# Optimization experiments

Measured on AMD Instinct MI355X. Metric: run time of the kernel, lower is better.

The kernel has to match this reference:

```python
import jax, jax.numpy as jnp
import numpy as np

B, E, F_DIM, D = 32, 16, 64, 512  # batch, extra dim, fea_dim, input_dim
EXP = 4                            # feed-forward expansion
EPS = 1e-5


def _layernorm(x, g, b):
    m = jnp.mean(x, axis=-1, keepdims=True)
    v = jnp.mean(jnp.square(x - m), axis=-1, keepdims=True)
    return (x - m) * jax.lax.rsqrt(v + EPS) * g + b


def setup_inputs() -> dict:
    key = jax.random.key(0)
    ks = jax.random.split(key, 12)
    s = 1.0 / np.sqrt(D)
    inp = {
        "x": jax.random.normal(ks[0], (B, E, F_DIM, D), jnp.float32),
        "ln1_g": jnp.ones((D,), jnp.float32),
        "ln1_b": jnp.zeros((D,), jnp.float32),
        "Wq": jax.random.uniform(ks[1], (D, D), jnp.float32, -s, s),
        "bq": jax.random.uniform(ks[2], (D,), jnp.float32, -s, s),
        "Wk": jax.random.uniform(ks[3], (D, D), jnp.float32, -s, s),
        "bk": jax.random.uniform(ks[4], (D,), jnp.float32, -s, s),
        "Wv": jax.random.uniform(ks[5], (D, D), jnp.float32, -s, s),
        "bv": jax.random.uniform(ks[6], (D,), jnp.float32, -s, s),
        "wn_g": jnp.ones((F_DIM,), jnp.float32),
        "wn_b": jnp.zeros((F_DIM,), jnp.float32),
        "ln2_g": jnp.ones((D,), jnp.float32),
        "ln2_b": jnp.zeros((D,), jnp.float32),
        "W1": jax.random.uniform(ks[7], (D, EXP * D), jnp.float32, -s, s),
        "b1": jax.random.uniform(ks[8], (EXP * D,), jnp.float32, -s, s),
        "W2": jax.random.uniform(ks[9], (EXP * D, D), jnp.float32, -1.0 / np.sqrt(EXP * D), 1.0 / np.sqrt(EXP * D)),
        "b2": jax.random.uniform(ks[10], (D,), jnp.float32, -1.0 / np.sqrt(EXP * D), 1.0 / np.sqrt(EXP * D)),
    }
    return inp


def reference(x, ln1_g, ln1_b, Wq, bq, Wk, bk, Wv, bv, wn_g, wn_b, ln2_g, ln2_b, W1, b1, W2, b2):
    # --- Residual 1: LN -> feature multi-head attention (dropout = identity) ---
    h = _layernorm(x, ln1_g, ln1_b)                       # [B,E,F,D]
    q = h @ Wq + bq
    k = h @ Wk + bk
    v = h @ Wv + bv
    energy = jnp.einsum('beqd,bekd->beqk', q, k)          # [B,E,F,F]
    # LayerNorm over the key axis of the raw scores (the fusion-breaking op)
    energy = _layernorm(energy, wn_g, wn_b)
    att = jax.nn.softmax(energy / jnp.sqrt(jnp.float32(D)), axis=-1)
    attn_out = jnp.einsum('beal,belv->beav', att, v)      # [B,E,F,D]
    x = x + attn_out
    # --- Residual 2: LN -> FFN (Linear -> Linear, no activation) ---
    h2 = _layernorm(x, ln2_g, ln2_b)
    ff = (h2 @ W1 + b1) @ W2 + b2
    return x + ff
```

## Files before the change

### kernel.cpp

```cpp
#include <hip/hip_runtime.h>
#include <hip/hip_bf16.h>


#define D_DIM 512
#define NROWS 32768
#define NBE   512

typedef __attribute__((ext_vector_type(8))) short bf16x8;
typedef __attribute__((ext_vector_type(4))) float f32x4;

typedef const __attribute__((address_space(1))) unsigned g_u32;
typedef __attribute__((address_space(3))) unsigned lds_u32;

__device__ __forceinline__ short f2bf(float f) {
  union { float f; unsigned u; } c; c.f = f;
  unsigned u = c.u;
  unsigned r = (u + 0x7FFFu + ((u >> 16) & 1u)) >> 16;
  return (short)r;
}
__device__ __forceinline__ float bf2f(short s) {
  union { unsigned u; float f; } c; c.u = ((unsigned)(unsigned short)s) << 16;
  return c.f;
}

__global__ __launch_bounds__(256) void wconvT(const float* __restrict__ W,
                                              short* __restrict__ Wt,
                                              int K, int N) {
  __shared__ float tile[32][33];
  const int t = threadIdx.x;
  const int r  = t >> 3;
  const int c4 = (t & 7) * 4;
  const long k0 = (long)blockIdx.y * 32;
  const long n0 = (long)blockIdx.x * 32;
  float4 v = *(const float4*)&W[(k0 + r) * N + n0 + c4];
  tile[r][c4 + 0] = v.x; tile[r][c4 + 1] = v.y;
  tile[r][c4 + 2] = v.z; tile[r][c4 + 3] = v.w;
  __syncthreads();
  union { short sh[4]; int2 v; } o;
#pragma unroll
  for (int j = 0; j < 4; ++j) o.sh[j] = f2bf(tile[c4 + j][r]);
  *(int2*)&Wt[(n0 + r) * K + k0 + c4] = o.v;
}

__global__ __launch_bounds__(256) void ln_kernel(const float* __restrict__ x,
                                                 const float* __restrict__ gam,
                                                 const float* __restrict__ bet,
                                                 short* __restrict__ h) {
  const int t = threadIdx.x;
  const long row = (long)blockIdx.x * 4 + (t >> 6);
  const int lane = t & 63;
  const float* xr = x + row * D_DIM + lane * 8;
  float4 a = *(const float4*)xr;
  float4 b = *(const float4*)(xr + 4);
  float xs[8] = {a.x, a.y, a.z, a.w, b.x, b.y, b.z, b.w};
  float s = 0.f, ss = 0.f;
#pragma unroll
  for (int j = 0; j < 8; ++j) { s += xs[j]; ss += xs[j] * xs[j]; }
#pragma unroll
  for (int m = 1; m < 64; m <<= 1) {
    s  += __shfl_xor(s, m);
    ss += __shfl_xor(ss, m);
  }
  float mean = s * (1.f / D_DIM);
  float var  = ss * (1.f / D_DIM) - mean * mean;
  float rstd = rsqrtf(var + 1e-5f);
  union { short sh[8]; int4 v; } o;
#pragma unroll
  for (int j = 0; j < 8; ++j) {
    int d = lane * 8 + j;
    o.sh[j] = f2bf((xs[j] - mean) * rstd * gam[d] + bet[d]);
  }
  *(int4*)&h[row * D_DIM + lane * 8] = o.v;
}

template <int OUT_BF16, int RESID>
__global__ __launch_bounds__(512, 2) void gemm256(
    const short* __restrict__ A, const short* __restrict__ Bt,
    const float* __restrict__ bias0, const float* __restrict__ bias1,
    const float* __restrict__ bias2,
    void* __restrict__ out0, void* __restrict__ out1, void* __restrict__ out2,
    const float* __restrict__ resid, int K, int nsplit) {
  extern __shared__ short smem[];
  short* As = smem;
  short* Bs = smem + 3 * 8192;

  const int t = threadIdx.x;
  const int wave = t >> 6, lane = t & 63;
  const int lr = lane & 15, g = lane >> 4;
  const int wr = wave >> 2, wc = wave & 3;

  const int gx = gridDim.x;
  const int nwg = gx * gridDim.y;
  const int hid = blockIdx.y * gx + blockIdx.x;
  const int lid = (hid & 7) * (nwg >> 3) + (hid >> 3);
  const int m0 = (lid / gx) * 256;
  const int n0 = (lid % gx) * 256;

  const int seg = n0 / nsplit;
  const int ncol0 = n0 - seg * nsplit;
  const float* bias = seg == 0 ? bias0 : (seg == 1 ? bias1 : bias2);
  void* outp = seg == 0 ? out0 : (seg == 1 ? out1 : out2);

  const int srow = lane & 15;
  const int scol = (lane >> 4) * 8;
  const short* gA0 = &A[(long)(m0 + wave * 32 + srow) * K + scol];
  const short* gB0 = &Bt[(long)(n0 + wave * 32 + srow) * K + scol];
  const long rstep = 16L * K;

#define STAGE_A(bufi, kk)                                                      \
  do {                                                                         \
    __builtin_amdgcn_global_load_lds((g_u32*)(gA0 + (kk)),                     \
        (lds_u32*)(As + (bufi) * 8192 + (wave * 2) * 512), 16, 0, 0);          \
    __builtin_amdgcn_global_load_lds((g_u32*)(gA0 + rstep + (kk)),             \
        (lds_u32*)(As + (bufi) * 8192 + (wave * 2 + 1) * 512), 16, 0, 0);      \
  } while (0)
#define STAGE_B(bufi, kk)                                                      \
  do {                                                                         \
    __builtin_amdgcn_global_load_lds((g_u32*)(gB0 + (kk)),                     \
        (lds_u32*)(Bs + (bufi) * 8192 + (wave * 2) * 512), 16, 0, 0);          \
    __builtin_amdgcn_global_load_lds((g_u32*)(gB0 + rstep + (kk)),             \
        (lds_u32*)(Bs + (bufi) * 8192 + (wave * 2 + 1) * 512), 16, 0, 0);      \
  } while (0)

  f32x4 acc[8][4];
  const f32x4 vzero = {0.f, 0.f, 0.f, 0.f};
#pragma unroll
  for (int mi = 0; mi < 8; ++mi)
#pragma unroll
    for (int ni = 0; ni < 4; ++ni) acc[mi][ni] = vzero;

  const int nt = K >> 5;
  STAGE_A(0, 0);  STAGE_B(0, 0);
  STAGE_A(1, 32); STAGE_B(1, 32);

  int cur = 0, stg = 2;
  const int fo = lane * 8;
  for (int T = 0; T < nt; ++T) {
    if (T < nt - 1) asm volatile("s_waitcnt vmcnt(4)" ::: "memory");
    else            asm volatile("s_waitcnt vmcnt(0)" ::: "memory");
    asm volatile("s_barrier" ::: "memory");

    const short* sA = As + cur * 8192;
    const short* sB = Bs + cur * 8192;
    const int kof = (T + 2) * 32;
    const bool stage_more = (T + 2 < nt);

    bf16x8 af[4], bfr[4];
#pragma unroll
    for (int i = 0; i < 4; ++i)
      af[i] = *(const bf16x8*)&sA[(wr * 8 + i) * 512 + fo];
#pragma unroll
    for (int i = 0; i < 4; ++i)
      bfr[i] = *(const bf16x8*)&sB[(wc * 4 + i) * 512 + fo];
    if (stage_more) STAGE_A(stg, kof);
    asm volatile("s_barrier" ::: "memory");
    __builtin_amdgcn_sched_barrier(0);
    __builtin_amdgcn_s_setprio(1);
#pragma unroll
    for (int mi = 0; mi < 4; ++mi)
#pragma unroll
      for (int ni = 0; ni < 4; ++ni)
        acc[mi][ni] = __builtin_amdgcn_mfma_f32_16x16x32_bf16(af[mi], bfr[ni], acc[mi][ni], 0, 0, 0);
    __builtin_amdgcn_s_setprio(0);
    __builtin_amdgcn_sched_barrier(0);
    asm volatile("s_barrier" ::: "memory");

#pragma unroll
    for (int i = 0; i < 4; ++i)
      af[i] = *(const bf16x8*)&sA[(wr * 8 + 4 + i) * 512 + fo];
    if (stage_more) STAGE_B(stg, kof);
    asm volatile("s_barrier" ::: "memory");
    __builtin_amdgcn_sched_barrier(0);
    __builtin_amdgcn_s_setprio(1);
#pragma unroll
    for (int mi = 0; mi < 4; ++mi)
#pragma unroll
      for (int ni = 0; ni < 4; ++ni)
        acc[4 + mi][ni] = __builtin_amdgcn_mfma_f32_16x16x32_bf16(af[mi], bfr[ni], acc[4 + mi][ni], 0, 0, 0);
    __builtin_amdgcn_s_setprio(0);
    __builtin_amdgcn_sched_barrier(0);

    cur = cur == 2 ? 0 : cur + 1;
    stg = stg == 2 ? 0 : stg + 1;
  }
#undef STAGE_A
#undef STAGE_B

#pragma unroll
  for (int ni = 0; ni < 4; ++ni) {
    const int col = ncol0 + wc * 64 + ni * 16 + lr;
    const float bv = bias[col];
#pragma unroll
    for (int mi = 0; mi < 8; ++mi) {
#pragma unroll
      for (int r = 0; r < 4; ++r) {
        const long row = m0 + wr * 128 + mi * 16 + g * 4 + r;
        float val = acc[mi][ni][r] + bv;
        if (RESID) val += resid[row * (long)nsplit + col];
        if (OUT_BF16) ((short*)outp)[row * (long)nsplit + col] = f2bf(val);
        else          ((float*)outp)[row * (long)nsplit + col] = val;
      }
    }
  }
}

__global__ __launch_bounds__(256) void attn_kernel(
    const short* __restrict__ q, const short* __restrict__ k,
    const short* __restrict__ v, const float* __restrict__ x,
    const float* __restrict__ wn_g, const float* __restrict__ wn_b,
    const float* __restrict__ ln2_g, const float* __restrict__ ln2_b,
    float* __restrict__ x1, short* __restrict__ h2) {
  __shared__ float att_s[64][68];
  const int t = threadIdx.x;
  const int wave = t >> 6, lane = t & 63;
  const int lr = lane & 15, g = lane >> 4;
  const long base = (long)blockIdx.x * 64;
  const long qoff = base * D_DIM;

  const f32x4 vzero = {0.f, 0.f, 0.f, 0.f};
  f32x4 acc[4];
#pragma unroll
  for (int nt = 0; nt < 4; ++nt) acc[nt] = vzero;

  for (int ks = 0; ks < 16; ++ks) {
    const int kc = ks * 32 + g * 8;
    bf16x8 afr = *(const bf16x8*)&q[qoff + (long)(wave * 16 + lr) * D_DIM + kc];
#pragma unroll
    for (int nt = 0; nt < 4; ++nt) {
      bf16x8 bfr = *(const bf16x8*)&k[qoff + (long)(nt * 16 + lr) * D_DIM + kc];
      acc[nt] = __builtin_amdgcn_mfma_f32_16x16x32_bf16(afr, bfr, acc[nt], 0, 0, 0);
    }
  }

  const float scale = 0.044194173824159216f;
#pragma unroll
  for (int r = 0; r < 4; ++r) {
    float s = 0.f, ss = 0.f;
#pragma unroll
    for (int nt = 0; nt < 4; ++nt) { float e = acc[nt][r]; s += e; ss += e * e; }
#pragma unroll
    for (int m = 1; m < 16; m <<= 1) { s += __shfl_xor(s, m); ss += __shfl_xor(ss, m); }
    float mean = s * (1.f / 64);
    float var  = ss * (1.f / 64) - mean * mean;
    float rstd = rsqrtf(var + 1e-5f);
    float e[4]; float mx = -1e30f;
#pragma unroll
    for (int nt = 0; nt < 4; ++nt) {
      int col = nt * 16 + lr;
      e[nt] = ((acc[nt][r] - mean) * rstd * wn_g[col] + wn_b[col]) * scale;
      mx = fmaxf(mx, e[nt]);
    }
#pragma unroll
    for (int m = 1; m < 16; m <<= 1) mx = fmaxf(mx, __shfl_xor(mx, m));
    float se = 0.f;
#pragma unroll
    for (int nt = 0; nt < 4; ++nt) { e[nt] = expf(e[nt] - mx); se += e[nt]; }
#pragma unroll
    for (int m = 1; m < 16; m <<= 1) se += __shfl_xor(se, m);
    float inv = 1.f / se;
#pragma unroll
    for (int nt = 0; nt < 4; ++nt)
      att_s[wave * 16 + 4 * g + r][nt * 16 + lr] = e[nt] * inv;
  }
  __syncthreads();

  const int d0 = lane * 8;
  float accp[16][8];
#pragma unroll
  for (int qi = 0; qi < 16; ++qi)
#pragma unroll
    for (int j = 0; j < 8; ++j) accp[qi][j] = 0.f;

  for (int kk0 = 0; kk0 < 64; kk0 += 4) {
    float vf[4][8];
#pragma unroll
    for (int kc = 0; kc < 4; ++kc) {
      bf16x8 vv = *(const bf16x8*)&v[qoff + (long)(kk0 + kc) * D_DIM + d0];
#pragma unroll
      for (int j = 0; j < 8; ++j) vf[kc][j] = bf2f(vv[j]);
    }
#pragma unroll
    for (int qi = 0; qi < 16; ++qi) {
      float4 a4 = *(const float4*)&att_s[wave * 16 + qi][kk0];
#pragma unroll
      for (int j = 0; j < 8; ++j) {
        accp[qi][j] += a4.x * vf[0][j];
        accp[qi][j] += a4.y * vf[1][j];
        accp[qi][j] += a4.z * vf[2][j];
        accp[qi][j] += a4.w * vf[3][j];
      }
    }
  }

  float g2v[8], b2v[8];
#pragma unroll
  for (int j = 0; j < 8; ++j) { g2v[j] = ln2_g[d0 + j]; b2v[j] = ln2_b[d0 + j]; }

#pragma unroll
  for (int qi = 0; qi < 16; ++qi) {
    const long row = base + wave * 16 + qi;
    const float* xr = x + row * D_DIM + d0;
    float4 x0 = *(const float4*)xr;
    float4 xb = *(const float4*)(xr + 4);
    accp[qi][0] += x0.x; accp[qi][1] += x0.y;
    accp[qi][2] += x0.z; accp[qi][3] += x0.w;
    accp[qi][4] += xb.x; accp[qi][5] += xb.y;
    accp[qi][6] += xb.z; accp[qi][7] += xb.w;
    float* po = x1 + row * D_DIM + d0;
    *(float4*)po       = make_float4(accp[qi][0], accp[qi][1], accp[qi][2], accp[qi][3]);
    *(float4*)(po + 4) = make_float4(accp[qi][4], accp[qi][5], accp[qi][6], accp[qi][7]);
    float s = 0.f, ss = 0.f;
#pragma unroll
    for (int j = 0; j < 8; ++j) { s += accp[qi][j]; ss += accp[qi][j] * accp[qi][j]; }
#pragma unroll
    for (int m = 1; m < 64; m <<= 1) { s += __shfl_xor(s, m); ss += __shfl_xor(ss, m); }
    float mean = s * (1.f / D_DIM);
    float var  = ss * (1.f / D_DIM) - mean * mean;
    float rstd = rsqrtf(var + 1e-5f);
    union { short sh[8]; int4 v; } o;
#pragma unroll
    for (int j = 0; j < 8; ++j)
      o.sh[j] = f2bf((accp[qi][j] - mean) * rstd * g2v[j] + b2v[j]);
    *(int4*)&h2[row * D_DIM + d0] = o.v;
  }
}

extern "C" void kernel_launch(void* const* d_in, const int* in_sizes, int n_in,
                              void* d_out, int out_size, void* d_ws, size_t ws_size,
                              hipStream_t stream) {
  (void)in_sizes; (void)n_in; (void)out_size; (void)ws_size;
  const float* x     = (const float*)d_in[0];
  const float* ln1_g = (const float*)d_in[1];
  const float* ln1_b = (const float*)d_in[2];
  const float* Wq    = (const float*)d_in[3];
  const float* bq    = (const float*)d_in[4];
  const float* Wk    = (const float*)d_in[5];
  const float* bk    = (const float*)d_in[6];
  const float* Wv    = (const float*)d_in[7];
  const float* bv    = (const float*)d_in[8];
  const float* wn_g  = (const float*)d_in[9];
  const float* wn_b  = (const float*)d_in[10];
  const float* ln2_g = (const float*)d_in[11];
  const float* ln2_b = (const float*)d_in[12];
  const float* W1    = (const float*)d_in[13];
  const float* b1    = (const float*)d_in[14];
  const float* W2    = (const float*)d_in[15];
  const float* b2    = (const float*)d_in[16];
  float* out = (float*)d_out;

  char* ws = (char*)d_ws;
  short* h   = (short*)(ws);
  short* qb  = (short*)(ws + (size_t)32  * 1024 * 1024);
  short* kb  = (short*)(ws + (size_t)64  * 1024 * 1024);
  short* vb  = (short*)(ws + (size_t)96  * 1024 * 1024);
  short* ff1 = (short*)(ws + (size_t)32  * 1024 * 1024);
  short* Wqt = (short*)(ws + (size_t)160 * 1024 * 1024);
  short* Wkt = Wqt + 512 * 512;
  short* Wvt = Wkt + 512 * 512;
  short* W1t = Wvt + 512 * 512;
  short* W2t = W1t + 512 * 2048;

  const size_t lds_bytes = 3 * 8192 * 2 * 2;
  (void)hipFuncSetAttribute((const void*)gemm256<1, 0>,
      hipFuncAttributeMaxDynamicSharedMemorySize, (int)lds_bytes);
  (void)hipFuncSetAttribute((const void*)gemm256<0, 1>,
      hipFuncAttributeMaxDynamicSharedMemorySize, (int)lds_bytes);

  wconvT<<<dim3(512 / 32, 512 / 32),  256, 0, stream>>>(Wq, Wqt, 512, 512);
  wconvT<<<dim3(512 / 32, 512 / 32),  256, 0, stream>>>(Wk, Wkt, 512, 512);
  wconvT<<<dim3(512 / 32, 512 / 32),  256, 0, stream>>>(Wv, Wvt, 512, 512);
  wconvT<<<dim3(2048 / 32, 512 / 32), 256, 0, stream>>>(W1, W1t, 512, 2048);
  wconvT<<<dim3(512 / 32, 2048 / 32), 256, 0, stream>>>(W2, W2t, 2048, 512);

  ln_kernel<<<NROWS / 4, 256, 0, stream>>>(x, ln1_g, ln1_b, h);

  dim3 gqkv(1536 / 256, NROWS / 256);
  gemm256<1, 0><<<gqkv, 512, lds_bytes, stream>>>(h, Wqt, bq, bk, bv,
                                                  qb, kb, vb, nullptr, 512, 512);

  attn_kernel<<<NBE, 256, 0, stream>>>(qb, kb, vb, x, wn_g, wn_b,
                                       ln2_g, ln2_b, out, h);

  dim3 gff1(2048 / 256, NROWS / 256);
  gemm256<1, 0><<<gff1, 512, lds_bytes, stream>>>(h, W1t, b1, b1, b1,
                                                  ff1, ff1, ff1, nullptr, 512, 2048);

  dim3 gff2(512 / 256, NROWS / 256);
  gemm256<0, 1><<<gff2, 512, lds_bytes, stream>>>(ff1, W2t, b2, b2, b2,
                                                  out, out, out, out, 2048, 512);
}
```

Measured before the change: 543.2 us.

## Simplify GEMM main loop to single-phase staging and vectorize epilogue via LDS

Restructures the GEMM K-loop so the next tile's A and B loads are issued together right after the barrier, and all 8x4 MFMAs run in one phase. This removes the interleaved half-tile barriers and setprio scheduling. The epilogue now stages each 16-row accumulator slab through per-wave LDS, so residual reads and output writes become contiguous 16-byte vector accesses instead of scattered scalar stores. The trade-off is more live fragment registers (8 A fragments), less fine-grained overlap of loads with MFMA, and a possible hazard: the staging loads are issued into buffer stg before other waves may have finished reading it.

```diff
diff --git a/kernel.cpp b/kernel.cpp
--- a/kernel.cpp
+++ b/kernel.cpp
@@ -140,45 +140,25 @@
     else            asm volatile("s_waitcnt vmcnt(0)" ::: "memory");
     asm volatile("s_barrier" ::: "memory");
 
+    if (T + 2 < nt) {
+      STAGE_A(stg, (T + 2) * 32);
+      STAGE_B(stg, (T + 2) * 32);
+    }
+
     const short* sA = As + cur * 8192;
     const short* sB = Bs + cur * 8192;
-    const int kof = (T + 2) * 32;
-    const bool stage_more = (T + 2 < nt);
-
-    bf16x8 af[4], bfr[4];
-#pragma unroll
-    for (int i = 0; i < 4; ++i)
+    bf16x8 af[8], bfr[4];
+#pragma unroll
+    for (int i = 0; i < 8; ++i)
       af[i] = *(const bf16x8*)&sA[(wr * 8 + i) * 512 + fo];
 #pragma unroll
     for (int i = 0; i < 4; ++i)
       bfr[i] = *(const bf16x8*)&sB[(wc * 4 + i) * 512 + fo];
-    if (stage_more) STAGE_A(stg, kof);
-    asm volatile("s_barrier" ::: "memory");
-    __builtin_amdgcn_sched_barrier(0);
-    __builtin_amdgcn_s_setprio(1);
-#pragma unroll
-    for (int mi = 0; mi < 4; ++mi)
+#pragma unroll
+    for (int mi = 0; mi < 8; ++mi)
 #pragma unroll
       for (int ni = 0; ni < 4; ++ni)
         acc[mi][ni] = __builtin_amdgcn_mfma_f32_16x16x32_bf16(af[mi], bfr[ni], acc[mi][ni], 0, 0, 0);
-    __builtin_amdgcn_s_setprio(0);
-    __builtin_amdgcn_sched_barrier(0);
-    asm volatile("s_barrier" ::: "memory");
-
-#pragma unroll
-    for (int i = 0; i < 4; ++i)
-      af[i] = *(const bf16x8*)&sA[(wr * 8 + 4 + i) * 512 + fo];
-    if (stage_more) STAGE_B(stg, kof);
-    asm volatile("s_barrier" ::: "memory");
-    __builtin_amdgcn_sched_barrier(0);
-    __builtin_amdgcn_s_setprio(1);
-#pragma unroll
-    for (int mi = 0; mi < 4; ++mi)
-#pragma unroll
-      for (int ni = 0; ni < 4; ++ni)
-        acc[4 + mi][ni] = __builtin_amdgcn_mfma_f32_16x16x32_bf16(af[mi], bfr[ni], acc[4 + mi][ni], 0, 0, 0);
-    __builtin_amdgcn_s_setprio(0);
-    __builtin_amdgcn_sched_barrier(0);
 
     cur = cur == 2 ? 0 : cur + 1;
     stg = stg == 2 ? 0 : stg + 1;
@@ -186,20 +166,52 @@
 #undef STAGE_A
 #undef STAGE_B
 
-#pragma unroll
-  for (int ni = 0; ni < 4; ++ni) {
-    const int col = ncol0 + wc * 64 + ni * 16 + lr;
-    const float bv = bias[col];
-#pragma unroll
-    for (int mi = 0; mi < 8; ++mi) {
-#pragma unroll
-      for (int r = 0; r < 4; ++r) {
-        const long row = m0 + wr * 128 + mi * 16 + g * 4 + r;
-        float val = acc[mi][ni][r] + bv;
-        if (RESID) val += resid[row * (long)nsplit + col];
-        if (OUT_BF16) ((short*)outp)[row * (long)nsplit + col] = f2bf(val);
-        else          ((float*)outp)[row * (long)nsplit + col] = val;
+  __syncthreads();
+  float* cs = (float*)smem + wave * 1088;
+  float bv[4];
+#pragma unroll
+  for (int ni = 0; ni < 4; ++ni) bv[ni] = bias[ncol0 + wc * 64 + ni * 16 + lr];
+  const int er = lane >> 2;
+  const int ec = (lane & 3) * 16;
+
+#pragma unroll
+  for (int mi = 0; mi < 8; ++mi) {
+#pragma unroll
+    for (int ni = 0; ni < 4; ++ni)
+#pragma unroll
+      for (int r = 0; r < 4; ++r)
+        cs[(g * 4 + r) * 68 + ni * 16 + lr] = acc[mi][ni][r] + bv[ni];
+    const long grow = m0 + wr * 128 + mi * 16 + er;
+    const long gcol = ncol0 + wc * 64 + ec;
+    float vals[16];
+#pragma unroll
+    for (int jb = 0; jb < 4; ++jb) {
+      float4 v = *(const float4*)&cs[er * 68 + ec + jb * 4];
+      vals[jb * 4 + 0] = v.x; vals[jb * 4 + 1] = v.y;
+      vals[jb * 4 + 2] = v.z; vals[jb * 4 + 3] = v.w;
+    }
+    if (RESID) {
+      const float* rp = resid + grow * (long)nsplit + gcol;
+#pragma unroll
+      for (int jb = 0; jb < 4; ++jb) {
+        float4 v = *(const float4*)&rp[jb * 4];
+        vals[jb * 4 + 0] += v.x; vals[jb * 4 + 1] += v.y;
+        vals[jb * 4 + 2] += v.z; vals[jb * 4 + 3] += v.w;
       }
+    }
+    if (OUT_BF16) {
+      union { short sh[16]; int4 q[2]; } o;
+#pragma unroll
+      for (int j = 0; j < 16; ++j) o.sh[j] = f2bf(vals[j]);
+      short* op = (short*)outp + grow * (long)nsplit + gcol;
+      *(int4*)op = o.q[0];
+      *(int4*)(op + 8) = o.q[1];
+    } else {
+      float* op = (float*)outp + grow * (long)nsplit + gcol;
+#pragma unroll
+      for (int jb = 0; jb < 4; ++jb)
+        *(float4*)&op[jb * 4] = make_float4(vals[jb * 4 + 0], vals[jb * 4 + 1],
+                                            vals[jb * 4 + 2], vals[jb * 4 + 3]);
     }
   }
 }
```

Result: faster. 507.8 us (-6.5%).
